# Optimization experiments

Hardware: AMD Instinct MI355X
Metric: run time of the kernel (lower is better)

Reference implementation:

```python
import jax, jax.numpy as jnp
import numpy as np

N_ATOMS = 100000
N_BONDS = 200001
ATOM_FDIM = 39
BOND_FDIM = 11
MAX_NB = 6
HIDDEN = 256
DEPTH = 6
N_MOLS = 2000
ATOMS_PER_MOL = N_ATOMS // N_MOLS


def setup_inputs() -> dict:
    key = jax.random.key(0)
    ks = jax.random.split(key, 8)
    fatoms = jax.random.uniform(ks[0], (N_ATOMS, ATOM_FDIM), dtype=jnp.float32)
    fbonds = jax.random.uniform(ks[1], (N_BONDS, ATOM_FDIM + BOND_FDIM), dtype=jnp.float32)
    agraph = jax.random.randint(ks[2], (N_ATOMS, MAX_NB), 0, N_BONDS, dtype=jnp.int32)
    bgraph = jax.random.randint(ks[3], (N_BONDS, MAX_NB), 0, N_BONDS, dtype=jnp.int32)
    starts = jnp.arange(N_MOLS, dtype=jnp.int32) * ATOMS_PER_MOL
    scope = jnp.stack([starts, jnp.full((N_MOLS,), ATOMS_PER_MOL, jnp.int32)], axis=1)
    s = 1.0 / np.sqrt(HIDDEN)
    W_i = jax.random.normal(ks[4], (HIDDEN, ATOM_FDIM + BOND_FDIM), dtype=jnp.float32) * s
    W_h = jax.random.normal(ks[5], (HIDDEN, HIDDEN), dtype=jnp.float32) * s
    W_o = jax.random.normal(ks[6], (HIDDEN, ATOM_FDIM + HIDDEN), dtype=jnp.float32) * s
    b_o = jax.random.normal(ks[7], (HIDDEN,), dtype=jnp.float32) * s
    return {"fatoms": fatoms, "fbonds": fbonds, "agraph": agraph,
            "bgraph": bgraph, "scope": scope, "W_i": W_i, "W_h": W_h,
            "W_o": W_o, "b_o": b_o}


def reference(fatoms, fbonds, agraph, bgraph, scope, W_i, W_h, W_o, b_o):
    # Initial bond messages: Linear (no bias) + ReLU
    binput = fbonds @ W_i.T                      # [B_bonds, H]
    message = jax.nn.relu(binput)
    # depth-1 rounds of gather -> sum over MAX_NB neighbors -> Linear -> ReLU + residual
    for _ in range(DEPTH - 1):
        nei = message[bgraph].sum(axis=1)        # [B_bonds, H]
        message = jax.nn.relu(binput + nei @ W_h.T)
    # Atom readout
    nei = message[agraph].sum(axis=1)            # [N_atoms, H]
    ainput = jnp.concatenate([fatoms, nei], axis=1)
    atom_hiddens = jax.nn.relu(ainput @ W_o.T + b_o)
    # Scope mean pooling: equal-size contiguous segments -> reshape-mean
    n_mols = scope.shape[0]
    mol_vecs = atom_hiddens.reshape(n_mols, -1, atom_hiddens.shape[-1]).mean(axis=1)
    return mol_vecs
```

## Files before the change

kernel.cpp:

```cpp
#include <hip/hip_runtime.h>
#include <hip/hip_bf16.h>

#define NB 200001
#define NA 100000
#define HID 256
#define AF 39
#define BFD 50
#define MAXNB 6
#define NMOL 2000
#define APM 50
#define KPAD 320

typedef __attribute__((ext_vector_type(8))) unsigned short ushort8;
typedef __attribute__((ext_vector_type(8))) short short8;
typedef __attribute__((ext_vector_type(4))) float f32x4;

__device__ __forceinline__ unsigned short f2b(float f) {
  __hip_bfloat16 h = __float2bfloat16(f);
  return *reinterpret_cast<unsigned short*>(&h);
}
__device__ __forceinline__ float b2f(unsigned short u) {
  union { unsigned int i; float f; } v; v.i = ((unsigned int)u) << 16; return v.f;
}

__global__ void prep_wc(const float* __restrict__ Wi, const float* __restrict__ Wh,
                        unsigned short* __restrict__ WcB) {
  int i = blockIdx.x * 256 + threadIdx.x;
  if (i >= HID * KPAD) return;
  int n = i / KPAD, k = i % KPAD;
  float v = 0.f;
  if (k < BFD) v = Wi[n * BFD + k];
  else if (k >= 64) v = Wh[n * HID + (k - 64)];
  WcB[i] = f2b(v);
}
__global__ void prep_wo(const float* __restrict__ Wo, unsigned short* __restrict__ WoP) {
  int i = blockIdx.x * 256 + threadIdx.x;
  if (i >= HID * KPAD) return;
  int n = i / KPAD, k = i % KPAD;
  float v = 0.f;
  if (k < AF) v = Wo[n * (AF + HID) + k];
  else if (k >= 64) v = Wo[n * (AF + HID) + AF + (k - 64)];
  WoP[i] = f2b(v);
}
__global__ void prep_fb(const float* __restrict__ fbonds, unsigned short* __restrict__ fbpad) {
  int i = blockIdx.x * 256 + threadIdx.x;
  if (i >= NB * 8) return;
  const int bond = i >> 3;
  const int c0 = (i & 7) * 8;
  ushort8 o;
  #pragma unroll
  for (int e = 0; e < 8; ++e) {
    const int c = c0 + e;
    o[e] = f2b(c < BFD ? fbonds[(size_t)bond * BFD + c] : 0.f);
  }
  *reinterpret_cast<ushort8*>(fbpad + (size_t)bond * 64 + c0) = o;
}

template <bool PREPPED>
__device__ __forceinline__ void stage_feat64(unsigned short (*As)[KPAD], int t, int b0,
                                             int nrows_total,
                                             const float* __restrict__ f32src, int f32dim, int realdim,
                                             const unsigned short* __restrict__ padsrc) {
  const int rs = t >> 3, csl = t & 7;
  #pragma unroll
  for (int it = 0; it < 2; ++it) {
    const int r = it * 32 + rs;
    const int row = b0 + r;
    const int c0 = csl * 8;
    ushort8 o;
    #pragma unroll
    for (int e = 0; e < 8; ++e) o[e] = 0;
    if (PREPPED) {
      if (row < nrows_total) o = *reinterpret_cast<const ushort8*>(padsrc + (size_t)row * 64 + c0);
    } else {
      #pragma unroll
      for (int e = 0; e < 8; ++e) {
        const int c = c0 + e;
        if (row < nrows_total && c < realdim) o[e] = f2b(f32src[(size_t)row * f32dim + c]);
      }
    }
    *reinterpret_cast<ushort8*>(&As[r][c0 ^ ((r & 7) << 3)]) = o;
  }
}

template <bool PREPPED>
__global__ __launch_bounds__(256, 4) void init_kernel(
    const float* __restrict__ fbonds, const unsigned short* __restrict__ fbpad,
    const unsigned short* __restrict__ WcB, unsigned short* __restrict__ msg0) {
  __shared__ unsigned short As[64][KPAD];
  const int t = threadIdx.x;
  const int b0 = blockIdx.x * 64;

  stage_feat64<PREPPED>(As, t, b0, NB, fbonds, BFD, BFD, fbpad);
  __syncthreads();

  const int w = t >> 6, lane = t & 63, lr = lane & 15, lg = lane >> 4;
  f32x4 acc[4][4];
  #pragma unroll
  for (int i = 0; i < 4; ++i)
    #pragma unroll
    for (int j = 0; j < 4; ++j) acc[i][j] = f32x4{0.f, 0.f, 0.f, 0.f};

  const unsigned short* wb[4];
  #pragma unroll
  for (int fn = 0; fn < 4; ++fn) wb[fn] = WcB + (size_t)(w * 64 + fn * 16 + lr) * KPAD;

  #pragma unroll
  for (int ks = 0; ks < 2; ++ks) {
    const int kb = ks * 32 + lg * 8;
    short8 a[4], b[4];
    #pragma unroll
    for (int fm = 0; fm < 4; ++fm) {
      const int m = fm * 16 + lr;
      a[fm] = *reinterpret_cast<const short8*>(&As[m][kb ^ ((m & 7) << 3)]);
    }
    #pragma unroll
    for (int fn = 0; fn < 4; ++fn)
      b[fn] = *reinterpret_cast<const short8*>(wb[fn] + kb);
    #pragma unroll
    for (int fm = 0; fm < 4; ++fm)
      #pragma unroll
      for (int fn = 0; fn < 4; ++fn)
        acc[fm][fn] = __builtin_amdgcn_mfma_f32_16x16x32_bf16(a[fm], b[fn], acc[fm][fn], 0, 0, 0);
  }

  #pragma unroll
  for (int fm = 0; fm < 4; ++fm)
    #pragma unroll
    for (int r = 0; r < 4; ++r) {
      const int m = fm * 16 + lg * 4 + r;
      const int bond = b0 + m;
      if (bond < NB) {
        #pragma unroll
        for (int fn = 0; fn < 4; ++fn) {
          const int col = w * 64 + fn * 16 + lr;
          msg0[(size_t)bond * HID + col] = f2b(fmaxf(acc[fm][fn][r], 0.f));
        }
      }
    }
}

template <bool PREPPED>
__global__ __launch_bounds__(256, 4) void round_kernel(
    const unsigned short* __restrict__ msg_in, unsigned short* __restrict__ msg_out,
    const float* __restrict__ fbonds, const unsigned short* __restrict__ fbpad,
    const unsigned short* __restrict__ WcB, const int* __restrict__ bgraph) {
  __shared__ unsigned short As[64][KPAD];
  const int t = threadIdx.x;
  const int b0 = blockIdx.x * 64;

  stage_feat64<PREPPED>(As, t, b0, NB, fbonds, BFD, BFD, fbpad);

  {
    const int rslot = t >> 5;
    const int c0 = (t & 31) * 8;
    #pragma unroll
    for (int it = 0; it < 8; ++it) {
      const int r = it * 8 + rslot;
      const int bond = b0 + r;
      float acc[8] = {0.f, 0.f, 0.f, 0.f, 0.f, 0.f, 0.f, 0.f};
      if (bond < NB) {
        const int* bg = bgraph + (size_t)bond * MAXNB;
        #pragma unroll
        for (int j = 0; j < MAXNB; ++j) {
          const int nb = bg[j];
          ushort8 v = *reinterpret_cast<const ushort8*>(msg_in + (size_t)nb * HID + c0);
          #pragma unroll
          for (int e = 0; e < 8; ++e) acc[e] += b2f(v[e]);
        }
      }
      ushort8 o;
      #pragma unroll
      for (int e = 0; e < 8; ++e) o[e] = f2b(acc[e]);
      const int cc = 64 + c0;
      *reinterpret_cast<ushort8*>(&As[r][cc ^ ((r & 7) << 3)]) = o;
    }
  }
  __syncthreads();

  const int w = t >> 6, lane = t & 63, lr = lane & 15, lg = lane >> 4;
  f32x4 acc[4][4];
  #pragma unroll
  for (int i = 0; i < 4; ++i)
    #pragma unroll
    for (int j = 0; j < 4; ++j) acc[i][j] = f32x4{0.f, 0.f, 0.f, 0.f};

  const unsigned short* wb[4];
  #pragma unroll
  for (int fn = 0; fn < 4; ++fn) wb[fn] = WcB + (size_t)(w * 64 + fn * 16 + lr) * KPAD;

  for (int kstep = 0; kstep < 5; ++kstep) {
    #pragma unroll
    for (int ks = 0; ks < 2; ++ks) {
      const int kb = ks * 32 + lg * 8;
      const int kA = kstep * 64 + kb;
      short8 a[4], b[4];
      #pragma unroll
      for (int fm = 0; fm < 4; ++fm) {
        const int m = fm * 16 + lr;
        a[fm] = *reinterpret_cast<const short8*>(&As[m][kA ^ ((m & 7) << 3)]);
      }
      #pragma unroll
      for (int fn = 0; fn < 4; ++fn)
        b[fn] = *reinterpret_cast<const short8*>(wb[fn] + kstep * 64 + kb);
      #pragma unroll
      for (int fm = 0; fm < 4; ++fm)
        #pragma unroll
        for (int fn = 0; fn < 4; ++fn)
          acc[fm][fn] = __builtin_amdgcn_mfma_f32_16x16x32_bf16(a[fm], b[fn], acc[fm][fn], 0, 0, 0);
    }
  }

  #pragma unroll
  for (int fm = 0; fm < 4; ++fm)
    #pragma unroll
    for (int r = 0; r < 4; ++r) {
      const int m = fm * 16 + lg * 4 + r;
      const int bond = b0 + m;
      if (bond < NB) {
        #pragma unroll
        for (int fn = 0; fn < 4; ++fn) {
          const int col = w * 64 + fn * 16 + lr;
          msg_out[(size_t)bond * HID + col] = f2b(fmaxf(acc[fm][fn][r], 0.f));
        }
      }
    }
}

__global__ __launch_bounds__(256, 4) void readout_kernel(
    const unsigned short* __restrict__ msg_in, const float* __restrict__ fatoms,
    const unsigned short* __restrict__ WoP, const float* __restrict__ b_o,
    const int* __restrict__ agraph, float* __restrict__ atomh) {
  __shared__ unsigned short As[64][KPAD];
  const int t = threadIdx.x;
  const int a0 = blockIdx.x * 64;

  stage_feat64<false>(As, t, a0, NA, fatoms, AF, AF, nullptr);

  {
    const int rslot = t >> 5;
    const int c0 = (t & 31) * 8;
    #pragma unroll
    for (int it = 0; it < 8; ++it) {
      const int r = it * 8 + rslot;
      const int atom = a0 + r;
      float acc[8] = {0.f, 0.f, 0.f, 0.f, 0.f, 0.f, 0.f, 0.f};
      if (atom < NA) {
        const int* ag = agraph + (size_t)atom * MAXNB;
        #pragma unroll
        for (int j = 0; j < MAXNB; ++j) {
          const int nb = ag[j];
          ushort8 v = *reinterpret_cast<const ushort8*>(msg_in + (size_t)nb * HID + c0);
          #pragma unroll
          for (int e = 0; e < 8; ++e) acc[e] += b2f(v[e]);
        }
      }
      ushort8 o;
      #pragma unroll
      for (int e = 0; e < 8; ++e) o[e] = f2b(acc[e]);
      const int cc = 64 + c0;
      *reinterpret_cast<ushort8*>(&As[r][cc ^ ((r & 7) << 3)]) = o;
    }
  }
  __syncthreads();

  const int w = t >> 6, lane = t & 63, lr = lane & 15, lg = lane >> 4;
  f32x4 acc[4][4];
  #pragma unroll
  for (int i = 0; i < 4; ++i)
    #pragma unroll
    for (int j = 0; j < 4; ++j) acc[i][j] = f32x4{0.f, 0.f, 0.f, 0.f};

  const unsigned short* wb[4];
  #pragma unroll
  for (int fn = 0; fn < 4; ++fn) wb[fn] = WoP + (size_t)(w * 64 + fn * 16 + lr) * KPAD;

  for (int kstep = 0; kstep < 5; ++kstep) {
    #pragma unroll
    for (int ks = 0; ks < 2; ++ks) {
      const int kb = ks * 32 + lg * 8;
      const int kA = kstep * 64 + kb;
      short8 a[4], b[4];
      #pragma unroll
      for (int fm = 0; fm < 4; ++fm) {
        const int m = fm * 16 + lr;
        a[fm] = *reinterpret_cast<const short8*>(&As[m][kA ^ ((m & 7) << 3)]);
      }
      #pragma unroll
      for (int fn = 0; fn < 4; ++fn)
        b[fn] = *reinterpret_cast<const short8*>(wb[fn] + kstep * 64 + kb);
      #pragma unroll
      for (int fm = 0; fm < 4; ++fm)
        #pragma unroll
        for (int fn = 0; fn < 4; ++fn)
          acc[fm][fn] = __builtin_amdgcn_mfma_f32_16x16x32_bf16(a[fm], b[fn], acc[fm][fn], 0, 0, 0);
    }
  }

  #pragma unroll
  for (int fm = 0; fm < 4; ++fm)
    #pragma unroll
    for (int r = 0; r < 4; ++r) {
      const int m = fm * 16 + lg * 4 + r;
      const int atom = a0 + m;
      if (atom < NA) {
        #pragma unroll
        for (int fn = 0; fn < 4; ++fn) {
          const int col = w * 64 + fn * 16 + lr;
          const float v = acc[fm][fn][r] + b_o[col];
          atomh[(size_t)atom * HID + col] = fmaxf(v, 0.f);
        }
      }
    }
}

__global__ __launch_bounds__(256) void pool_kernel(const float* __restrict__ atomh,
                                                   float* __restrict__ out) {
  const int mol = blockIdx.x;
  const int t = threadIdx.x;
  const float* base = atomh + (size_t)mol * APM * HID + t;
  float s = 0.f;
  #pragma unroll 5
  for (int i = 0; i < APM; ++i) s += base[(size_t)i * HID];
  out[(size_t)mol * HID + t] = s * (1.f / APM);
}

extern "C" void kernel_launch(void* const* d_in, const int* in_sizes, int n_in,
                              void* d_out, int out_size, void* d_ws, size_t ws_size,
                              hipStream_t stream) {
  const float* fatoms = (const float*)d_in[0];
  const float* fbonds = (const float*)d_in[1];
  const int* agraph = (const int*)d_in[2];
  const int* bgraph = (const int*)d_in[3];
  const float* W_i = (const float*)d_in[5];
  const float* W_h = (const float*)d_in[6];
  const float* W_o = (const float*)d_in[7];
  const float* b_o = (const float*)d_in[8];

  char* ws = (char*)d_ws;
  size_t off = 0;
  auto alloc = [&](size_t bytes) {
    void* p = ws + off;
    off += (bytes + 255) & ~(size_t)255;
    return p;
  };
  unsigned short* msgA = (unsigned short*)alloc((size_t)NB * HID * 2);
  unsigned short* msgB = (unsigned short*)alloc((size_t)NB * HID * 2);
  unsigned short* WcB = (unsigned short*)alloc((size_t)HID * KPAD * 2);
  unsigned short* WoP = (unsigned short*)alloc((size_t)HID * KPAD * 2);
  const size_t base_need = off;
  unsigned short* fbpad = (unsigned short*)alloc((size_t)NB * 64 * 2);
  const size_t fb_need = off;
  float* atomh = (float*)msgA;

  if (ws_size < base_need) return;
  const bool prepped = (ws_size >= fb_need);

  prep_wc<<<(HID * KPAD + 255) / 256, 256, 0, stream>>>(W_i, W_h, WcB);
  prep_wo<<<(HID * KPAD + 255) / 256, 256, 0, stream>>>(W_o, WoP);
  if (prepped)
    prep_fb<<<(NB * 8 + 255) / 256, 256, 0, stream>>>(fbonds, fbpad);

  const int nblk_b = (NB + 63) / 64;
  if (prepped)
    init_kernel<true><<<nblk_b, 256, 0, stream>>>(fbonds, fbpad, WcB, msgA);
  else
    init_kernel<false><<<nblk_b, 256, 0, stream>>>(fbonds, fbpad, WcB, msgA);

  unsigned short* src = msgA;
  unsigned short* dst = msgB;
  for (int d = 0; d < 5; ++d) {
    if (prepped)
      round_kernel<true><<<nblk_b, 256, 0, stream>>>(src, dst, fbonds, fbpad, WcB, bgraph);
    else
      round_kernel<false><<<nblk_b, 256, 0, stream>>>(src, dst, fbonds, fbpad, WcB, bgraph);
    unsigned short* tmp = src; src = dst; dst = tmp;
  }

  const int nblk_a = (NA + 63) / 64;
  readout_kernel<<<nblk_a, 256, 0, stream>>>(src, fatoms, WoP, b_o, agraph, atomh);
  pool_kernel<<<NMOL, 256, 0, stream>>>(atomh, (float*)d_out);
}
```

Before: 946.3 us.

## Halve row tile to 32, stage neighbor indices in LDS, batch gather loads

Shrinks the per-block row tile from 64 to 32 rows in the init, round and readout kernels, which halves LDS use and lets occupancy rise (launch bounds go from 4 to 5 blocks). Neighbor indices are now preloaded into shared memory first. Each thread then issues all six neighbor row loads before summing them, which is meant to expose more memory-level parallelism in the latency-bound gather. The cost is that weight B-fragments are reread from global/L2 twice as often per output row, and there is an extra barrier.

```diff
diff --git a/kernel.cpp b/kernel.cpp
--- a/kernel.cpp
+++ b/kernel.cpp
@@ -10,6 +10,7 @@
 #define NMOL 2000
 #define APM 50
 #define KPAD 320
+#define BM 32
 
 typedef __attribute__((ext_vector_type(8))) unsigned short ushort8;
 typedef __attribute__((ext_vector_type(8))) short short8;
@@ -57,47 +58,73 @@
 }
 
 template <bool PREPPED>
-__device__ __forceinline__ void stage_feat64(unsigned short (*As)[KPAD], int t, int b0,
+__device__ __forceinline__ void stage_feat32(unsigned short (*As)[KPAD], int t, int b0,
                                              int nrows_total,
                                              const float* __restrict__ f32src, int f32dim, int realdim,
                                              const unsigned short* __restrict__ padsrc) {
-  const int rs = t >> 3, csl = t & 7;
-  #pragma unroll
-  for (int it = 0; it < 2; ++it) {
-    const int r = it * 32 + rs;
+  const int r = t >> 3;
+  const int c0 = (t & 7) * 8;
+  const int row = b0 + r;
+  ushort8 o;
+  #pragma unroll
+  for (int e = 0; e < 8; ++e) o[e] = 0;
+  if (PREPPED) {
+    if (row < nrows_total) o = *reinterpret_cast<const ushort8*>(padsrc + (size_t)row * 64 + c0);
+  } else {
+    #pragma unroll
+    for (int e = 0; e < 8; ++e) {
+      const int c = c0 + e;
+      if (row < nrows_total && c < realdim) o[e] = f2b(f32src[(size_t)row * f32dim + c]);
+    }
+  }
+  *reinterpret_cast<ushort8*>(&As[r][c0 ^ ((r & 7) << 3)]) = o;
+}
+
+__device__ __forceinline__ void gather32(unsigned short (*As)[KPAD], const int (*sidx)[MAXNB],
+                                         int t, int b0, int nrows_total,
+                                         const unsigned short* __restrict__ msg_in) {
+  const int rslot = t >> 5;
+  const int c0 = (t & 31) * 8;
+  #pragma unroll
+  for (int it = 0; it < 4; ++it) {
+    const int r = it * 8 + rslot;
     const int row = b0 + r;
-    const int c0 = csl * 8;
+    float acc[8] = {0.f, 0.f, 0.f, 0.f, 0.f, 0.f, 0.f, 0.f};
+    if (row < nrows_total) {
+      ushort8 v[MAXNB];
+      #pragma unroll
+      for (int j = 0; j < MAXNB; ++j) {
+        const int nb = sidx[r][j];
+        v[j] = *reinterpret_cast<const ushort8*>(msg_in + (size_t)nb * HID + c0);
+      }
+      #pragma unroll
+      for (int j = 0; j < MAXNB; ++j)
+        #pragma unroll
+        for (int e = 0; e < 8; ++e) acc[e] += b2f(v[j][e]);
+    }
     ushort8 o;
     #pragma unroll
-    for (int e = 0; e < 8; ++e) o[e] = 0;
-    if (PREPPED) {
-      if (row < nrows_total) o = *reinterpret_cast<const ushort8*>(padsrc + (size_t)row * 64 + c0);
-    } else {
-      #pragma unroll
-      for (int e = 0; e < 8; ++e) {
-        const int c = c0 + e;
-        if (row < nrows_total && c < realdim) o[e] = f2b(f32src[(size_t)row * f32dim + c]);
-      }
-    }
-    *reinterpret_cast<ushort8*>(&As[r][c0 ^ ((r & 7) << 3)]) = o;
+    for (int e = 0; e < 8; ++e) o[e] = f2b(acc[e]);
+    const int cc = 64 + c0;
+    *reinterpret_cast<ushort8*>(&As[r][cc ^ ((r & 7) << 3)]) = o;
   }
 }
 
 template <bool PREPPED>
-__global__ __launch_bounds__(256, 4) void init_kernel(
+__global__ __launch_bounds__(256, 5) void init_kernel(
     const float* __restrict__ fbonds, const unsigned short* __restrict__ fbpad,
     const unsigned short* __restrict__ WcB, unsigned short* __restrict__ msg0) {
-  __shared__ unsigned short As[64][KPAD];
+  __shared__ unsigned short As[BM][KPAD];
   const int t = threadIdx.x;
-  const int b0 = blockIdx.x * 64;
-
-  stage_feat64<PREPPED>(As, t, b0, NB, fbonds, BFD, BFD, fbpad);
+  const int b0 = blockIdx.x * BM;
+
+  stage_feat32<PREPPED>(As, t, b0, NB, fbonds, BFD, BFD, fbpad);
   __syncthreads();
 
   const int w = t >> 6, lane = t & 63, lr = lane & 15, lg = lane >> 4;
-  f32x4 acc[4][4];
-  #pragma unroll
-  for (int i = 0; i < 4; ++i)
+  f32x4 acc[2][4];
+  #pragma unroll
+  for (int i = 0; i < 2; ++i)
     #pragma unroll
     for (int j = 0; j < 4; ++j) acc[i][j] = f32x4{0.f, 0.f, 0.f, 0.f};
 
@@ -108,9 +135,9 @@
   #pragma unroll
   for (int ks = 0; ks < 2; ++ks) {
     const int kb = ks * 32 + lg * 8;
-    short8 a[4], b[4];
-    #pragma unroll
-    for (int fm = 0; fm < 4; ++fm) {
+    short8 a[2], b[4];
+    #pragma unroll
+    for (int fm = 0; fm < 2; ++fm) {
       const int m = fm * 16 + lr;
       a[fm] = *reinterpret_cast<const short8*>(&As[m][kb ^ ((m & 7) << 3)]);
     }
@@ -118,14 +145,14 @@
     for (int fn = 0; fn < 4; ++fn)
       b[fn] = *reinterpret_cast<const short8*>(wb[fn] + kb);
     #pragma unroll
-    for (int fm = 0; fm < 4; ++fm)
+    for (int fm = 0; fm < 2; ++fm)
       #pragma unroll
       for (int fn = 0; fn < 4; ++fn)
         acc[fm][fn] = __builtin_amdgcn_mfma_f32_16x16x32_bf16(a[fm], b[fn], acc[fm][fn], 0, 0, 0);
   }
 
   #pragma unroll
-  for (int fm = 0; fm < 4; ++fm)
+  for (int fm = 0; fm < 2; ++fm)
     #pragma unroll
     for (int r = 0; r < 4; ++r) {
       const int m = fm * 16 + lg * 4 + r;
@@ -141,47 +168,30 @@
 }
 
 template <bool PREPPED>
-__global__ __launch_bounds__(256, 4) void round_kernel(
+__global__ __launch_bounds__(256, 5) void round_kernel(
     const unsigned short* __restrict__ msg_in, unsigned short* __restrict__ msg_out,
     const float* __restrict__ fbonds, const unsigned short* __restrict__ fbpad,
     const unsigned short* __restrict__ WcB, const int* __restrict__ bgraph) {
-  __shared__ unsigned short As[64][KPAD];
+  __shared__ unsigned short As[BM][KPAD];
+  __shared__ int sidx[BM][MAXNB];
   const int t = threadIdx.x;
-  const int b0 = blockIdx.x * 64;
-
-  stage_feat64<PREPPED>(As, t, b0, NB, fbonds, BFD, BFD, fbpad);
-
-  {
-    const int rslot = t >> 5;
-    const int c0 = (t & 31) * 8;
-    #pragma unroll
-    for (int it = 0; it < 8; ++it) {
-      const int r = it * 8 + rslot;
-      const int bond = b0 + r;
-      float acc[8] = {0.f, 0.f, 0.f, 0.f, 0.f, 0.f, 0.f, 0.f};
-      if (bond < NB) {
-        const int* bg = bgraph + (size_t)bond * MAXNB;
-        #pragma unroll
-        for (int j = 0; j < MAXNB; ++j) {
-          const int nb = bg[j];
-          ushort8 v = *reinterpret_cast<const ushort8*>(msg_in + (size_t)nb * HID + c0);
-          #pragma unroll
-          for (int e = 0; e < 8; ++e) acc[e] += b2f(v[e]);
-        }
-      }
-      ushort8 o;
-      #pragma unroll
-      for (int e = 0; e < 8; ++e) o[e] = f2b(acc[e]);
-      const int cc = 64 + c0;
-      *reinterpret_cast<ushort8*>(&As[r][cc ^ ((r & 7) << 3)]) = o;
-    }
-  }
+  const int b0 = blockIdx.x * BM;
+
+  if (t < BM * MAXNB) {
+    const int r = t / MAXNB, j = t % MAXNB;
+    const int bond = b0 + r;
+    sidx[r][j] = (bond < NB) ? bgraph[(size_t)bond * MAXNB + j] : 0;
+  }
+  stage_feat32<PREPPED>(As, t, b0, NB, fbonds, BFD, BFD, fbpad);
+  __syncthreads();
+
+  gather32(As, sidx, t, b0, NB, msg_in);
   __syncthreads();
 
   const int w = t >> 6, lane = t & 63, lr = lane & 15, lg = lane >> 4;
-  f32x4 acc[4][4];
-  #pragma unroll
-  for (int i = 0; i < 4; ++i)
+  f32x4 acc[2][4];
+  #pragma unroll
+  for (int i = 0; i < 2; ++i)
     #pragma unroll
     for (int j = 0; j < 4; ++j) acc[i][j] = f32x4{0.f, 0.f, 0.f, 0.f};
 
@@ -194,9 +204,9 @@
     for (int ks = 0; ks < 2; ++ks) {
       const int kb = ks * 32 + lg * 8;
       const int kA = kstep * 64 + kb;
-      short8 a[4], b[4];
-      #pragma unroll
-      for (int fm = 0; fm < 4; ++fm) {
+      short8 a[2], b[4];
+      #pragma unroll
+      for (int fm = 0; fm < 2; ++fm) {
         const int m = fm * 16 + lr;
         a[fm] = *reinterpret_cast<const short8*>(&As[m][kA ^ ((m & 7) << 3)]);
       }
@@ -204,7 +214,7 @@
       for (int fn = 0; fn < 4; ++fn)
         b[fn] = *reinterpret_cast<const short8*>(wb[fn] + kstep * 64 + kb);
       #pragma unroll
-      for (int fm = 0; fm < 4; ++fm)
+      for (int fm = 0; fm < 2; ++fm)
         #pragma unroll
         for (int fn = 0; fn < 4; ++fn)
           acc[fm][fn] = __builtin_amdgcn_mfma_f32_16x16x32_bf16(a[fm], b[fn], acc[fm][fn], 0, 0, 0);
@@ -212,7 +222,7 @@
   }
 
   #pragma unroll
-  for (int fm = 0; fm < 4; ++fm)
+  for (int fm = 0; fm < 2; ++fm)
     #pragma unroll
     for (int r = 0; r < 4; ++r) {
       const int m = fm * 16 + lg * 4 + r;
@@ -227,47 +237,30 @@
     }
 }
 
-__global__ __launch_bounds__(256, 4) void readout_kernel(
+__global__ __launch_bounds__(256, 5) void readout_kernel(
     const unsigned short* __restrict__ msg_in, const float* __restrict__ fatoms,
     const unsigned short* __restrict__ WoP, const float* __restrict__ b_o,
     const int* __restrict__ agraph, float* __restrict__ atomh) {
-  __shared__ unsigned short As[64][KPAD];
+  __shared__ unsigned short As[BM][KPAD];
+  __shared__ int sidx[BM][MAXNB];
   const int t = threadIdx.x;
-  const int a0 = blockIdx.x * 64;
-
-  stage_feat64<false>(As, t, a0, NA, fatoms, AF, AF, nullptr);
-
-  {
-    const int rslot = t >> 5;
-    const int c0 = (t & 31) * 8;
-    #pragma unroll
-    for (int it = 0; it < 8; ++it) {
-      const int r = it * 8 + rslot;
-      const int atom = a0 + r;
-      float acc[8] = {0.f, 0.f, 0.f, 0.f, 0.f, 0.f, 0.f, 0.f};
-      if (atom < NA) {
-        const int* ag = agraph + (size_t)atom * MAXNB;
-        #pragma unroll
-        for (int j = 0; j < MAXNB; ++j) {
-          const int nb = ag[j];
-          ushort8 v = *reinterpret_cast<const ushort8*>(msg_in + (size_t)nb * HID + c0);
-          #pragma unroll
-          for (int e = 0; e < 8; ++e) acc[e] += b2f(v[e]);
-        }
-      }
-      ushort8 o;
-      #pragma unroll
-      for (int e = 0; e < 8; ++e) o[e] = f2b(acc[e]);
-      const int cc = 64 + c0;
-      *reinterpret_cast<ushort8*>(&As[r][cc ^ ((r & 7) << 3)]) = o;
-    }
-  }
+  const int a0 = blockIdx.x * BM;
+
+  if (t < BM * MAXNB) {
+    const int r = t / MAXNB, j = t % MAXNB;
+    const int atom = a0 + r;
+    sidx[r][j] = (atom < NA) ? agraph[(size_t)atom * MAXNB + j] : 0;
+  }
+  stage_feat32<false>(As, t, a0, NA, fatoms, AF, AF, nullptr);
+  __syncthreads();
+
+  gather32(As, sidx, t, a0, NA, msg_in);
   __syncthreads();
 
   const int w = t >> 6, lane = t & 63, lr = lane & 15, lg = lane >> 4;
-  f32x4 acc[4][4];
-  #pragma unroll
-  for (int i = 0; i < 4; ++i)
+  f32x4 acc[2][4];
+  #pragma unroll
+  for (int i = 0; i < 2; ++i)
     #pragma unroll
     for (int j = 0; j < 4; ++j) acc[i][j] = f32x4{0.f, 0.f, 0.f, 0.f};
 
@@ -280,9 +273,9 @@
     for (int ks = 0; ks < 2; ++ks) {
       const int kb = ks * 32 + lg * 8;
       const int kA = kstep * 64 + kb;
-      short8 a[4], b[4];
-      #pragma unroll
-      for (int fm = 0; fm < 4; ++fm) {
+      short8 a[2], b[4];
+      #pragma unroll
+      for (int fm = 0; fm < 2; ++fm) {
         const int m = fm * 16 + lr;
         a[fm] = *reinterpret_cast<const short8*>(&As[m][kA ^ ((m & 7) << 3)]);
       }
@@ -290,7 +283,7 @@
       for (int fn = 0; fn < 4; ++fn)
         b[fn] = *reinterpret_cast<const short8*>(wb[fn] + kstep * 64 + kb);
       #pragma unroll
-      for (int fm = 0; fm < 4; ++fm)
+      for (int fm = 0; fm < 2; ++fm)
         #pragma unroll
         for (int fn = 0; fn < 4; ++fn)
           acc[fm][fn] = __builtin_amdgcn_mfma_f32_16x16x32_bf16(a[fm], b[fn], acc[fm][fn], 0, 0, 0);
@@ -298,7 +291,7 @@
   }
 
   #pragma unroll
-  for (int fm = 0; fm < 4; ++fm)
+  for (int fm = 0; fm < 2; ++fm)
     #pragma unroll
     for (int r = 0; r < 4; ++r) {
       const int m = fm * 16 + lg * 4 + r;
@@ -361,7 +354,7 @@
   if (prepped)
     prep_fb<<<(NB * 8 + 255) / 256, 256, 0, stream>>>(fbonds, fbpad);
 
-  const int nblk_b = (NB + 63) / 64;
+  const int nblk_b = (NB + BM - 1) / BM;
   if (prepped)
     init_kernel<true><<<nblk_b, 256, 0, stream>>>(fbonds, fbpad, WcB, msgA);
   else
@@ -377,7 +370,7 @@
     unsigned short* tmp = src; src = dst; dst = tmp;
   }
 
-  const int nblk_a = (NA + 63) / 64;
+  const int nblk_a = (NA + BM - 1) / BM;
   readout_kernel<<<nblk_a, 256, 0, stream>>>(src, fatoms, WoP, b_o, agraph, atomh);
   pool_kernel<<<NMOL, 256, 0, stream>>>(atomh, (float*)d_out);
 }
```

Result: slower. 1.056 ms (+11.6%).
